# Optimization experiments

Measured on AMD Instinct MI355X. Metric: run time of the kernel, lower is better.

## Reference

```python
import jax, jax.numpy as jnp
import numpy as np

T = 8
TAU = 2.0
V_TH = 1.0
ALPHA = 2.0  # ATan surrogate alpha (spikingjelly default)

@jax.custom_vjp
def spike_fn(x):
    # Heaviside forward, ATan surrogate backward
    return (x >= 0.0).astype(x.dtype)

def _spike_fwd(x):
    return spike_fn(x), x

def _spike_bwd(x, g):
    sg = (ALPHA / 2.0) / (1.0 + (jnp.pi / 2.0 * ALPHA * x) ** 2)
    return (g * sg,)

spike_fn.defvjp(_spike_fwd, _spike_bwd)

def lif_scan(currents):
    """LIF over time. currents: (T, B, D). tau=2, v_reset=0 (hard), decay_input=True, detach_reset=True."""
    v0 = jnp.zeros(currents.shape[1:], currents.dtype)
    def step(v, x):
        v = v + (x - v) / TAU            # charge with input decay
        s = spike_fn(v - V_TH)           # fire
        sd = jax.lax.stop_gradient(s)    # detach_reset=True
        v = v * (1.0 - sd)               # hard reset to v_reset=0
        return v, s
    _, spikes = jax.lax.scan(step, v0, currents)
    return spikes  # (T, B, D)

def _linear(x, W, b):
    # x: (T,B,I), W: (O,I) torch layout
    return jnp.einsum('tbi,oi->tbo', x, W) + b

def setup_inputs() -> dict:
    key = jax.random.key(0)
    ks = jax.random.split(key, 9)
    B, D_in, D_out = 32768, 128, 64
    def lin(k, o, i):
        k1, k2 = jax.random.split(k)
        bound = 1.0 / np.sqrt(i)
        W = jax.random.uniform(k1, (o, i), jnp.float32, -bound, bound)
        b = jax.random.uniform(k2, (o,), jnp.float32, -bound, bound)
        return W, b
    W1, b1 = lin(ks[1], 256, D_in)
    W2, b2 = lin(ks[2], 128, 256)
    W3, b3 = lin(ks[3], 64, 128)
    W4, b4 = lin(ks[4], D_out, 64)
    x = jax.random.normal(ks[0], (B, D_in), jnp.float32)
    return {"x": x, "W1": W1, "b1": b1, "W2": W2, "b2": b2,
            "W3": W3, "b3": b3, "W4": W4, "b4": b4}

def reference(x, W1, b1, W2, b2, W3, b3, W4, b4):
    # Poisson rate coding: bernoulli(sigmoid(x)) per timestep (fixed key => deterministic)
    p = jax.nn.sigmoid(x)
    enc_key = jax.random.key(42)
    spikes_in = jax.random.bernoulli(enc_key, p, (T,) + x.shape).astype(x.dtype)  # (T,B,128)
    h = lif_scan(_linear(spikes_in, W1, b1))
    h = lif_scan(_linear(h, W2, b2))
    h = lif_scan(_linear(h, W3, b3))
    out = _linear(h, W4, b4)  # (T,B,64)
    return out.mean(axis=0)   # (B,64)
```

## Files before the change

### kernel.cpp

```cpp
#include <hip/hip_runtime.h>
#include <hip/hip_bf16.h>
#include <stdint.h>
#include <math.h>

#define TT 8

typedef __attribute__((ext_vector_type(8))) short short8;
typedef __attribute__((ext_vector_type(4))) float f32x4;

__device__ __forceinline__ uint16_t bf16_rne(float f) {
  uint32_t u = __float_as_uint(f);
  return (uint16_t)((u + 0x7fffu + ((u >> 16) & 1u)) >> 16);
}
__device__ __forceinline__ float bf16_f32(uint16_t b) {
  return __uint_as_float((uint32_t)b << 16);
}

__device__ __forceinline__ uint32_t rotl32(uint32_t v, int r) {
#if __has_builtin(__builtin_amdgcn_alignbit)
  return __builtin_amdgcn_alignbit(v, v, 32 - r);
#else
  return (v << r) | (v >> (32 - r));
#endif
}

__device__ __forceinline__ void tf_0_42(uint32_t x0, uint32_t x1,
                                        uint32_t& o0, uint32_t& o1) {
  const uint32_t K1 = 42u, KS2 = 0x1BD11BDAu ^ 42u;
  uint32_t v0 = x0;
  uint32_t v1 = x1 + K1;
#define R4(a,b,c,d) \
  v0 += v1; v1 = rotl32(v1, a); v1 ^= v0; \
  v0 += v1; v1 = rotl32(v1, b); v1 ^= v0; \
  v0 += v1; v1 = rotl32(v1, c); v1 ^= v0; \
  v0 += v1; v1 = rotl32(v1, d); v1 ^= v0;
  R4(13, 15, 26, 6)   v0 += K1;  v1 += KS2 + 1u;
  R4(17, 29, 16, 24)  v0 += KS2; v1 += 2u;
  R4(13, 15, 26, 6)   v1 += K1 + 3u;
  R4(17, 29, 16, 24)  v0 += K1;  v1 += KS2 + 4u;
  R4(13, 15, 26, 6)   v0 += KS2; v1 += 5u;
#undef R4
  o0 = v0; o1 = v1;
}

__device__ __forceinline__ void threefry2x32(uint32_t k0, uint32_t k1,
                                             uint32_t x0, uint32_t x1,
                                             uint32_t& o0, uint32_t& o1) {
  const uint32_t ks2 = 0x1BD11BDAu ^ k0 ^ k1;
  uint32_t v0 = x0 + k0, v1 = x1 + k1;
#define TFR(r) { v0 += v1; v1 = rotl32(v1, r); v1 ^= v0; }
  TFR(13) TFR(15) TFR(26) TFR(6)   v0 += k1;  v1 += ks2 + 1u;
  TFR(17) TFR(29) TFR(16) TFR(24)  v0 += ks2; v1 += k0 + 2u;
  TFR(13) TFR(15) TFR(26) TFR(6)   v0 += k0;  v1 += k1 + 3u;
  TFR(17) TFR(29) TFR(16) TFR(24)  v0 += k1;  v1 += ks2 + 4u;
  TFR(13) TFR(15) TFR(26) TFR(6)   v0 += ks2; v1 += k0 + 5u;
#undef TFR
  o0 = v0; o1 = v1;
}

__device__ __forceinline__ bool bern_lt(uint32_t bits, float p32, float xv) {
  const float u = __uint_as_float((bits >> 9) | 0x3f800000u) - 1.0f;
  const float d = u - p32;
  if (__builtin_expect(fabsf(d) < 8e-6f, 0)) {
    const double p = 1.0 / (1.0 + exp(-(double)xv));
    return (double)u < p;
  }
  return d < 0.0f;
}

__global__ void __launch_bounds__(256)
w1split_kernel(const float* __restrict__ W1, uint16_t* __restrict__ W1s)
{
  const int gid = blockIdx.x * 256 + threadIdx.x;
  const int j = gid & 7, nt = (gid >> 3) & 1, lane = (gid >> 4) & 63;
  const int sp = (gid >> 10) & 3, nc = gid >> 12;
  const int k = sp * 32 + (lane >> 4) * 8 + j;
  const int n = nc * 32 + nt * 16 + (lane & 15);
  W1s[gid] = bf16_rne(W1[n * 128 + k]);
}

__global__ void __launch_bounds__(256, 6)
snn_k1(const float* __restrict__ x, const uint16_t* __restrict__ W1s,
       const float* __restrict__ B1, const float* __restrict__ B4,
       uint32_t* __restrict__ s1g, uint32_t* __restrict__ flgg,
       float* __restrict__ out)
{
  __shared__ __align__(16) uint8_t sbits[128 * 16];
  __shared__ float bias_s[256];
  __shared__ uint16_t s1t[128 * 16];
  __shared__ uint32_t exc;

  const int tid = threadIdx.x;
  const int lane = tid & 63, wid = tid >> 6, g = lane >> 4;

  for (int i = tid; i < 1024; i += 256) ((uint32_t*)s1t)[i] = 0;
  if (tid == 0) exc = 0;
  bias_s[tid] = B1[tid];

  {
    const int b = tid >> 4, w8 = tid & 15;
    const int gb = blockIdx.x * 16 + b;
    float xv[8];
    *(float4*)&xv[0] = *(const float4*)&x[(size_t)gb * 128 + w8 * 8];
    *(float4*)&xv[4] = *(const float4*)&x[(size_t)gb * 128 + w8 * 8 + 4];
    const uint32_t ebase = ((uint32_t)gb << 7) | (uint32_t)(w8 * 8);
    uint32_t m[TT] = {0, 0, 0, 0, 0, 0, 0, 0};
    uint32_t ambig = 0;
    #pragma unroll
    for (int j = 0; j < 8; ++j) {
      const float p1 = 1.0f + 1.0f / (1.0f + expf(-xv[j]));
      uint32_t T = (__float_as_uint(p1) & 0x7fffffu) << 9;
      if (p1 >= 2.0f) T = 0xFFFFFFFFu;
      #pragma unroll
      for (int t = 0; t < 4; ++t) {
        const uint32_t e = ebase + (uint32_t)j + ((uint32_t)t << 22);
        uint32_t o0, o1;
        tf_0_42(e, e + 0x01000000u, o0, o1);
        m[t]     |= (o0 < T ? 1u : 0u) << j;
        m[t + 4] |= (o1 < T ? 1u : 0u) << j;
        const uint32_t a0 = o0 - T + 43008u, a1 = o1 - T + 43008u;
        ambig |= ((a0 < 86016u) || (a1 < 86016u)) ? (1u << j) : 0u;
      }
    }
    if (__builtin_expect(ambig != 0u, 0)) {
      for (int j = 0; j < 8; ++j) {
        if ((ambig >> j) & 1u) {
          const double p = 1.0 / (1.0 + exp(-(double)xv[j]));
          for (int t = 0; t < 4; ++t) {
            const uint32_t e = ebase + (uint32_t)j + ((uint32_t)t << 22);
            uint32_t o0, o1;
            tf_0_42(e, e + 0x01000000u, o0, o1);
            const float u0 = __uint_as_float((o0 >> 9) | 0x3f800000u) - 1.0f;
            const float u1 = __uint_as_float((o1 >> 9) | 0x3f800000u) - 1.0f;
            m[t]     = (m[t]     & ~(1u << j)) | (((double)u0 < p ? 1u : 0u) << j);
            m[t + 4] = (m[t + 4] & ~(1u << j)) | (((double)u1 < p ? 1u : 0u) << j);
          }
        }
      }
    }
    #pragma unroll
    for (int t = 0; t < TT; ++t)
      sbits[(b * 8 + t) * 16 + w8] = (uint8_t)m[t];
  }
  __syncthreads();

  short8 a0_0, a0_1, a0_2, a0_3, a1_0, a1_1, a1_2, a1_3;
  {
    const uint8_t* rp0 = &sbits[(wid * 32 + (lane & 15)) * 16];
    const uint8_t* rp1 = rp0 + 256;
#define MKFRAG(dst, rp, s) { \
    const uint32_t byte = (rp)[(s) * 4 + g]; \
    short8 a; \
    a[0] = (short)((byte & 1u)   ? 0x3F80 : 0); \
    a[1] = (short)((byte & 2u)   ? 0x3F80 : 0); \
    a[2] = (short)((byte & 4u)   ? 0x3F80 : 0); \
    a[3] = (short)((byte & 8u)   ? 0x3F80 : 0); \
    a[4] = (short)((byte & 16u)  ? 0x3F80 : 0); \
    a[5] = (short)((byte & 32u)  ? 0x3F80 : 0); \
    a[6] = (short)((byte & 64u)  ? 0x3F80 : 0); \
    a[7] = (short)((byte & 128u) ? 0x3F80 : 0); \
    dst = a; }
    MKFRAG(a0_0, rp0, 0) MKFRAG(a0_1, rp0, 1) MKFRAG(a0_2, rp0, 2) MKFRAG(a0_3, rp0, 3)
    MKFRAG(a1_0, rp1, 0) MKFRAG(a1_1, rp1, 1) MKFRAG(a1_2, rp1, 2) MKFRAG(a1_3, rp1, 3)
#undef MKFRAG
  }

  const uint8_t* wlane = (const uint8_t*)W1s + lane * 32;

  #pragma unroll 1
  for (int nc = 0; nc < 8; ++nc) {
    const uint8_t* wnc = wlane + nc * 8192;
    f32x4 C00 = {0.f, 0.f, 0.f, 0.f};
    f32x4 C01 = C00, C10 = C00, C11 = C00;
    short8 bf0, bf1;
#define STEP(sp, A0, A1) \
    bf0 = *(const short8*)(wnc + (sp) * 2048); \
    bf1 = *(const short8*)(wnc + (sp) * 2048 + 16); \
    C00 = __builtin_amdgcn_mfma_f32_16x16x32_bf16(A0, bf0, C00, 0, 0, 0); \
    C10 = __builtin_amdgcn_mfma_f32_16x16x32_bf16(A1, bf0, C10, 0, 0, 0); \
    C01 = __builtin_amdgcn_mfma_f32_16x16x32_bf16(A0, bf1, C01, 0, 0, 0); \
    C11 = __builtin_amdgcn_mfma_f32_16x16x32_bf16(A1, bf1, C11, 0, 0, 0);
    STEP(0, a0_0, a1_0) STEP(1, a0_1, a1_1) STEP(2, a0_2, a1_2) STEP(3, a0_3, a1_3)
#undef STEP

#define EPI(Cv, mi, nt) { \
    const float bbv = bias_s[nc * 32 + (nt) * 16 + (lane & 15)]; \
    const float cr0 = Cv[0] + bbv, cr1 = Cv[1] + bbv; \
    const float cr2 = Cv[2] + bbv, cr3 = Cv[3] + bbv; \
    float u = cr0 * 0.5f; \
    float mx = u; \
    u = (u + cr1) * 0.5f; mx = fmaxf(mx, u); \
    u = (u + cr2) * 0.5f; mx = fmaxf(mx, u); \
    u = (u + cr3) * 0.5f; mx = fmaxf(mx, u); \
    const float u3o = __shfl_xor(u, 16); \
    const float ub = (g & 1) ? mx + fmaxf(u3o, 0.f) * 0.5f : mx; \
    if (__any(ub >= 1.0f)) { \
      float v = 0.f; uint32_t nib = 0; \
      { const float vn = (v + cr0) * 0.5f; const bool s = vn >= 1.0f; nib |= s ? 1u : 0u; v = s ? 0.f : vn; } \
      { const float vn = (v + cr1) * 0.5f; const bool s = vn >= 1.0f; nib |= s ? 2u : 0u; v = s ? 0.f : vn; } \
      { const float vn = (v + cr2) * 0.5f; const bool s = vn >= 1.0f; nib |= s ? 4u : 0u; v = s ? 0.f : vn; } \
      { const float vn = (v + cr3) * 0.5f; const bool s = vn >= 1.0f; nib |= s ? 8u : 0u; v = s ? 0.f : vn; } \
      const float v3 = __shfl_xor(v, 16); \
      if (g & 1) { \
        v = v3; nib = 0; \
        { const float vn = (v + cr0) * 0.5f; const bool s = vn >= 1.0f; nib |= s ? 1u : 0u; v = s ? 0.f : vn; } \
        { const float vn = (v + cr1) * 0.5f; const bool s = vn >= 1.0f; nib |= s ? 2u : 0u; v = s ? 0.f : vn; } \
        { const float vn = (v + cr2) * 0.5f; const bool s = vn >= 1.0f; nib |= s ? 4u : 0u; v = s ? 0.f : vn; } \
        { const float vn = (v + cr3) * 0.5f; const bool s = vn >= 1.0f; nib |= s ? 8u : 0u; v = s ? 0.f : vn; } \
      } \
      _Pragma("unroll") \
      for (int r = 0; r < 4; ++r) { \
        const unsigned long long bal = __ballot((nib >> r) & 1u); \
        if ((lane & 15) == 0) { \
          const uint16_t w16v = (uint16_t)((bal >> (g * 16)) & 0xffffu); \
          if (w16v) { \
            const int row = wid * 32 + (mi) * 16 + g * 4 + r; \
            s1t[row * 16 + nc * 2 + (nt)] = w16v; \
          } \
        } \
      } \
    } }
    EPI(C00, 0, 0) EPI(C01, 0, 1) EPI(C10, 1, 0) EPI(C11, 1, 1)
#undef EPI
  }

  __syncthreads();
  if (tid < 128) {
    const uint32_t* rp = (const uint32_t*)&s1t[tid * 16];
    int c = 0;
    #pragma unroll
    for (int j = 0; j < 8; ++j) c += __popc(rp[j]);
    if (c >= 15) atomicOr(&exc, 1u);
  }
  ((uint4*)s1g)[(size_t)blockIdx.x * 256 + tid] = ((const uint4*)s1t)[tid];
  __syncthreads();
  const uint32_t e = exc;
  if (tid == 0) flgg[blockIdx.x] = e;
  if (!e) {
    const float4 bv = *reinterpret_cast<const float4*>(&B4[(tid & 15) * 4]);
    float* op = &out[(size_t)(blockIdx.x * 16 + (tid >> 4)) * 64 + (tid & 15) * 4];
    *reinterpret_cast<float4*>(op) = bv;
  }
}

template<int I, int O, bool LAST>
__device__ __forceinline__ void layer_valu(
    const float* __restrict__ Wg, const float* __restrict__ Bg,
    const uint32_t* __restrict__ s_in, uint8_t* __restrict__ s_out,
    uint32_t* __restrict__ flg_next,
    float* __restrict__ wbuf, float* __restrict__ bias_s,
    float* __restrict__ outp, int bglob0, uint32_t msk)
{
  constexpr int WST = 66;
  const int tid = threadIdx.x;
  const int b  = tid >> 3;
  const int oc = tid & 7;
  __syncthreads();
  if (tid < O) bias_s[tid] = Bg[tid];

  for (int q = 0; q < O / 64; ++q) {
    const int obase = q * 64;
    float acc[TT][8];
    #pragma unroll
    for (int t = 0; t < TT; ++t)
      #pragma unroll
      for (int j = 0; j < 8; ++j) acc[t][j] = 0.f;

    for (int ic = 0; ic < I / 64; ++ic) {
      if (!((msk >> ic) & 1u)) continue;
      __syncthreads();
      #pragma unroll
      for (int k = 0; k < 4; ++k) {
        int fi = tid + k * 256;
        int o  = fi >> 4;
        int i4 = fi & 15;
        const float4 w4 = *reinterpret_cast<const float4*>(
            &Wg[(size_t)(obase + o) * I + ic * 64 + i4 * 4]);
        float* wp = &wbuf[(i4 * 4) * WST + o];
        wp[0 * WST] = w4.x; wp[1 * WST] = w4.y;
        wp[2 * WST] = w4.z; wp[3 * WST] = w4.w;
      }
      __syncthreads();
      uint32_t r[TT][2];
      uint32_t any = 0;
      #pragma unroll
      for (int t = 0; t < TT; ++t) {
        const uint32_t* sp = &s_in[(size_t)(b * 8 + t) * (I / 32) + ic * 2];
        r[t][0] = sp[0]; r[t][1] = sp[1];
        any |= r[t][0] | r[t][1];
      }
      if (any) {
        #pragma unroll
        for (int w = 0; w < 2; ++w) {
          for (int i2 = 0; i2 < 32; ++i2) {
            const float* wrow = &wbuf[(w * 32 + i2) * WST + oc * 8];
            const float2 wa = *reinterpret_cast<const float2*>(wrow);
            const float2 wb = *reinterpret_cast<const float2*>(wrow + 2);
            const float2 wc = *reinterpret_cast<const float2*>(wrow + 4);
            const float2 wd = *reinterpret_cast<const float2*>(wrow + 6);
            #pragma unroll
            for (int t = 0; t < TT; ++t) {
              const float sf = (float)((r[t][w] >> i2) & 1u);
              acc[t][0] += wa.x * sf; acc[t][1] += wa.y * sf;
              acc[t][2] += wb.x * sf; acc[t][3] += wb.y * sf;
              acc[t][4] += wc.x * sf; acc[t][5] += wc.y * sf;
              acc[t][6] += wd.x * sf; acc[t][7] += wd.y * sf;
            }
          }
        }
      }
    }
    if constexpr (!LAST) {
      float v[8];
      #pragma unroll
      for (int j = 0; j < 8; ++j) v[j] = 0.f;
      #pragma unroll
      for (int t = 0; t < TT; ++t) {
        uint32_t m = 0;
        #pragma unroll
        for (int j = 0; j < 8; ++j) {
          const float cur = acc[t][j] + bias_s[obase + oc * 8 + j];
          const float vn = (v[j] + cur) * 0.5f;
          const bool s = vn >= 1.0f;
          m |= (uint32_t)s << j;
          v[j] = s ? 0.0f : vn;
        }
        if (m) {
          const int byi = (obase >> 3) + oc;
          s_out[(size_t)(b * 8 + t) * (O / 8) + byi] = (uint8_t)m;
          atomicOr(flg_next, 1u << (byi >> 3));
        }
      }
    } else {
      float oacc[8];
      #pragma unroll
      for (int j = 0; j < 8; ++j) oacc[j] = 0.f;
      #pragma unroll
      for (int t = 0; t < TT; ++t)
        #pragma unroll
        for (int j = 0; j < 8; ++j) oacc[j] += acc[t][j];
      float4 o0, o1;
      o0.x = oacc[0] * 0.125f + bias_s[oc * 8 + 0];
      o0.y = oacc[1] * 0.125f + bias_s[oc * 8 + 1];
      o0.z = oacc[2] * 0.125f + bias_s[oc * 8 + 2];
      o0.w = oacc[3] * 0.125f + bias_s[oc * 8 + 3];
      o1.x = oacc[4] * 0.125f + bias_s[oc * 8 + 4];
      o1.y = oacc[5] * 0.125f + bias_s[oc * 8 + 5];
      o1.z = oacc[6] * 0.125f + bias_s[oc * 8 + 6];
      o1.w = oacc[7] * 0.125f + bias_s[oc * 8 + 7];
      float* op = &outp[(size_t)(bglob0 + b) * 64 + oc * 8];
      *reinterpret_cast<float4*>(op)     = o0;
      *reinterpret_cast<float4*>(op + 4) = o1;
    }
  }
}

__global__ void __launch_bounds__(256, 4)
snn_k2(const uint32_t* __restrict__ s1g, const uint32_t* __restrict__ flgg,
       const float* __restrict__ W2, const float* __restrict__ B2,
       const float* __restrict__ W3, const float* __restrict__ B3,
       const float* __restrict__ W4, const float* __restrict__ B4,
       float* __restrict__ out)
{
  const uint32_t m1 = flgg[2 * blockIdx.x] | flgg[2 * blockIdx.x + 1];
  if (!m1) return;

  __shared__ __align__(16) uint8_t smem[32272];
  float*    wbuf   = (float*)smem;
  float*    bias_s = (float*)(smem + 16896);
  uint8_t*  s2     = smem + 17920;
  uint32_t* s1     = (uint32_t*)(smem + 22016);
  uint8_t*  s3     = smem + 30208;
  uint32_t* flg    = (uint32_t*)(smem + 32256);

  const int tid = threadIdx.x;
  const int bglob0 = blockIdx.x * 32;

  ((uint4*)s1)[tid]       = ((const uint4*)s1g)[(size_t)blockIdx.x * 512 + tid];
  ((uint4*)s1)[tid + 256] = ((const uint4*)s1g)[(size_t)blockIdx.x * 512 + tid + 256];
  for (int i = tid; i < 1024; i += 256) ((uint32_t*)s2)[i] = 0;
  for (int i = tid; i < 516;  i += 256) ((uint32_t*)s3)[i] = 0;

  layer_valu<256, 128, false>(W2, B2, s1, s2, &flg[1],
                              wbuf, bias_s, nullptr, bglob0, 0xFu);
  __syncthreads();
  const uint32_t m2 = flg[1];
  if (m2)
    layer_valu<128, 64, false>(W3, B3, (const uint32_t*)s2, s3, &flg[2],
                               wbuf, bias_s, nullptr, bglob0, m2);
  __syncthreads();
  const uint32_t m3 = flg[2];
  if (m3) {
    layer_valu<64, 64, true>(W4, B4, (const uint32_t*)s3, nullptr, nullptr,
                             wbuf, bias_s, out, bglob0, m3);
  } else {
    const int b = tid >> 3, oc = tid & 7;
    const float4 b0 = *reinterpret_cast<const float4*>(&B4[oc * 8]);
    const float4 b1 = *reinterpret_cast<const float4*>(&B4[oc * 8 + 4]);
    float* op = &out[(size_t)(bglob0 + b) * 64 + oc * 8];
    *reinterpret_cast<float4*>(op)     = b0;
    *reinterpret_cast<float4*>(op + 4) = b1;
  }
}

__global__ void __launch_bounds__(256, 4)
snn_fb(const float* __restrict__ x,
       const float* __restrict__ W1, const float* __restrict__ B1,
       const float* __restrict__ W2, const float* __restrict__ B2,
       const float* __restrict__ W3, const float* __restrict__ B3,
       const float* __restrict__ W4, const float* __restrict__ B4,
       float* __restrict__ out)
{
  __shared__ __align__(16) uint8_t smem[32272];
  uint16_t* B_lds  = (uint16_t*)smem;
  float*    wbuf   = (float*)smem;
  float*    bias_s = (float*)(smem + 16896);
  uint32_t* s0     = (uint32_t*)(smem + 17920);
  uint8_t*  s2     = smem + 17920;
  uint16_t* s1     = (uint16_t*)(smem + 22016);
  uint8_t*  s3     = smem + 30208;
  uint32_t* flg    = (uint32_t*)(smem + 32256);

  const int tid = threadIdx.x;
  const int lane = tid & 63, wid = tid >> 6;
  const int bglob0 = blockIdx.x * 32;

  for (int i = tid; i < 2564; i += 256)
    ((uint32_t*)(smem + 22016))[i] = 0;

  {
    const int b = tid >> 3, w16 = tid & 7;
    const int gb = bglob0 + b;
    float xv[16];
    #pragma unroll
    for (int k = 0; k < 4; ++k)
      *(float4*)&xv[k * 4] =
          *(const float4*)&x[(size_t)gb * 128 + w16 * 16 + k * 4];
    uint32_t m[TT] = {0, 0, 0, 0, 0, 0, 0, 0};
    for (int j = 0; j < 16; ++j) {
      const int d = w16 * 16 + j;
      const float p32 = 1.0f / (1.0f + expf(-xv[j]));
      #pragma unroll
      for (int t = 0; t < 4; ++t) {
        const uint32_t e = ((uint32_t)t << 22) | ((uint32_t)gb << 7) | (uint32_t)d;
        uint32_t o0, o1;
        threefry2x32(0u, 42u, e, e + 0x01000000u, o0, o1);
        m[t]     |= (uint32_t)bern_lt(o0, p32, xv[j]) << j;
        m[t + 4] |= (uint32_t)bern_lt(o1, p32, xv[j]) << j;
      }
    }
    #pragma unroll
    for (int t = 0; t < TT; ++t)
      ((uint16_t*)s0)[(b * 8 + t) * 8 + w16] = (uint16_t)m[t];
  }
  bias_s[tid] = B1[tid];
  __syncthreads();

  short8 afrag[4][4];
  #pragma unroll
  for (int m = 0; m < 4; ++m) {
    const int row = wid * 64 + m * 16 + (lane & 15);
    #pragma unroll
    for (int s = 0; s < 4; ++s) {
      const uint32_t wrd = s0[row * 4 + s];
      const uint32_t byte = (wrd >> ((lane >> 4) * 8)) & 0xffu;
      short8 a;
      #pragma unroll
      for (int j = 0; j < 8; ++j)
        a[j] = (short)(((byte >> j) & 1u) ? 0x3F80 : 0);
      afrag[m][s] = a;
    }
  }
  __syncthreads();
  for (int i = tid; i < 1024; i += 256)
    ((uint32_t*)s2)[i] = 0;

  for (int nc = 0; nc < 8; ++nc) {
    __syncthreads();
    {
      const int col = tid >> 3, kq = tid & 7;
      const float* wsrc = &W1[(size_t)(nc * 32 + col) * 128 + kq * 16];
      float4 f[4];
      #pragma unroll
      for (int k = 0; k < 4; ++k)
        f[k] = *reinterpret_cast<const float4*>(wsrc + k * 4);
      #pragma unroll
      for (int h = 0; h < 2; ++h) {
        const int k0 = kq * 16 + h * 8;
        const int sp = k0 >> 5, gg = (k0 >> 3) & 3;
        short8 hv, lv;
        #pragma unroll
        for (int e = 0; e < 8; ++e) {
          const float w = ((const float*)&f[2 * h])[e];
          const uint16_t hb = bf16_rne(w);
          const uint16_t lb = bf16_rne(w - bf16_f32(hb));
          hv[e] = (short)hb; lv[e] = (short)lb;
        }
        *(short8*)(B_lds + ((sp * 4 + gg) * 33 + col) * 8)       = hv;
        *(short8*)(B_lds + (((sp + 4) * 4 + gg) * 33 + col) * 8) = lv;
      }
    }
    __syncthreads();
    f32x4 C[4][2];
    #pragma unroll
    for (int m = 0; m < 4; ++m)
      #pragma unroll
      for (int nt = 0; nt < 2; ++nt)
        C[m][nt] = (f32x4){0.f, 0.f, 0.f, 0.f};
    #pragma unroll
    for (int nt = 0; nt < 2; ++nt)
      #pragma unroll
      for (int sp = 0; sp < 8; ++sp) {
        const short8 bf = *(const short8*)(
            B_lds + ((sp * 4 + (lane >> 4)) * 33 + nt * 16 + (lane & 15)) * 8);
        #pragma unroll
        for (int m = 0; m < 4; ++m)
          C[m][nt] = __builtin_amdgcn_mfma_f32_16x16x32_bf16(
              afrag[m][sp & 3], bf, C[m][nt], 0, 0, 0);
      }
    const int g = lane >> 4;
    #pragma unroll
    for (int m = 0; m < 4; ++m)
      #pragma unroll
      for (int nt = 0; nt < 2; ++nt) {
        const float bb = bias_s[nc * 32 + nt * 16 + (lane & 15)];
        const float c0 = C[m][nt][0] + bb, c1 = C[m][nt][1] + bb;
        const float c2 = C[m][nt][2] + bb, c3 = C[m][nt][3] + bb;
        const float mxc = fmaxf(fmaxf(c0, c1), fmaxf(c2, c3));
        if (__any(mxc >= 1.0f)) {
          float cr[4] = {c0, c1, c2, c3};
          float v = 0.f; uint32_t nib = 0;
          #pragma unroll
          for (int r = 0; r < 4; ++r) {
            const float vn = (v + cr[r]) * 0.5f;
            const bool s = vn >= 1.0f;
            nib |= (uint32_t)s << r;
            v = s ? 0.f : vn;
          }
          const float v3 = __shfl_xor(v, 16);
          if (g & 1) {
            v = v3; nib = 0;
            #pragma unroll
            for (int r = 0; r < 4; ++r) {
              const float vn = (v + cr[r]) * 0.5f;
              const bool s = vn >= 1.0f;
              nib |= (uint32_t)s << r;
              v = s ? 0.f : vn;
            }
          }
          #pragma unroll
          for (int r = 0; r < 4; ++r) {
            const unsigned long long bal = __ballot((nib >> r) & 1u);
            if ((lane & 15) == 0) {
              const uint16_t w16v = (uint16_t)((bal >> (g * 16)) & 0xffffu);
              if (w16v) {
                const int row = wid * 64 + m * 16 + g * 4 + r;
                const int wds = nc * 2 + nt;
                s1[row * 16 + wds] = w16v;
                atomicOr(&flg[0], 1u << (wds >> 2));
              }
            }
          }
        }
      }
  }

  __syncthreads();
  const uint32_t m1 = flg[0];
  if (m1)
    layer_valu<256, 128, false>(W2, B2, (const uint32_t*)s1, s2, &flg[1],
                                wbuf, bias_s, nullptr, bglob0, m1);
  __syncthreads();
  const uint32_t m2 = flg[1];
  if (m2)
    layer_valu<128, 64, false>(W3, B3, (const uint32_t*)s2, s3, &flg[2],
                               wbuf, bias_s, nullptr, bglob0, m2);
  __syncthreads();
  const uint32_t m3 = flg[2];
  if (m3) {
    layer_valu<64, 64, true>(W4, B4, (const uint32_t*)s3, nullptr, nullptr,
                             wbuf, bias_s, out, bglob0, m3);
  } else {
    const int b = tid >> 3, oc = tid & 7;
    const float4 b0 = *reinterpret_cast<const float4*>(&B4[oc * 8]);
    const float4 b1 = *reinterpret_cast<const float4*>(&B4[oc * 8 + 4]);
    float* op = &out[(size_t)(bglob0 + b) * 64 + oc * 8];
    *reinterpret_cast<float4*>(op)     = b0;
    *reinterpret_cast<float4*>(op + 4) = b1;
  }
}

extern "C" void kernel_launch(void* const* d_in, const int* in_sizes, int n_in,
                              void* d_out, int out_size, void* d_ws, size_t ws_size,
                              hipStream_t stream) {
  const float* x  = (const float*)d_in[0];
  const float* W1 = (const float*)d_in[1];
  const float* B1 = (const float*)d_in[2];
  const float* W2 = (const float*)d_in[3];
  const float* B2 = (const float*)d_in[4];
  const float* W3 = (const float*)d_in[5];
  const float* B3 = (const float*)d_in[6];
  const float* W4 = (const float*)d_in[7];
  const float* B4 = (const float*)d_in[8];
  float* out = (float*)d_out;
  const size_t s1_bytes  = (size_t)262144 * 32;
  const size_t flg_bytes = 2048 * 4;
  const size_t w1s_bytes = 32768 * 2;
  if (ws_size >= s1_bytes + flg_bytes + w1s_bytes) {
    uint32_t* s1g  = (uint32_t*)d_ws;
    uint32_t* flgg = (uint32_t*)((uint8_t*)d_ws + s1_bytes);
    uint16_t* W1s  = (uint16_t*)((uint8_t*)d_ws + s1_bytes + flg_bytes);
    hipLaunchKernelGGL(w1split_kernel, dim3(128), dim3(256), 0, stream, W1, W1s);
    hipLaunchKernelGGL(snn_k1, dim3(2048), dim3(256), 0, stream,
                       x, W1s, B1, B4, s1g, flgg, out);
    hipLaunchKernelGGL(snn_k2, dim3(1024), dim3(256), 0, stream,
                       s1g, flgg, W2, B2, W3, B3, W4, B4, out);
  } else {
    hipLaunchKernelGGL(snn_fb, dim3(1024), dim3(256), 0, stream,
                       x, W1, B1, W2, B2, W3, B3, W4, B4, out);
  }
}
```

Before: 77.39 us.

## Make snn_k1 wave-independent with register bpermute fragments and per-wave flags

Rewrites the first kernel so each wavefront handles its own 4 batch rows end to end. Bernoulli spike masks stay in registers and are redistributed into MFMA A-fragments with ds_bpermute instead of going through shared memory. The block-wide syncs and shared atomic for the overflow flag are replaced by a per-wave ballot and a per-wave flag array, which snn_k2 now ORs over 8 entries. Work is also remapped so each lane handles 32 inputs at one timestep pair, __expf replaces expf, and the occupancy hint drops from 6 to 4 blocks, which may reduce latency hiding.

```diff
diff --git a/kernel.cpp b/kernel.cpp
--- a/kernel.cpp
+++ b/kernel.cpp
@@ -79,77 +79,76 @@
   W1s[gid] = bf16_rne(W1[n * 128 + k]);
 }
 
-__global__ void __launch_bounds__(256, 6)
+__global__ void __launch_bounds__(256, 4)
 snn_k1(const float* __restrict__ x, const uint16_t* __restrict__ W1s,
        const float* __restrict__ B1, const float* __restrict__ B4,
        uint32_t* __restrict__ s1g, uint32_t* __restrict__ flgg,
        float* __restrict__ out)
 {
-  __shared__ __align__(16) uint8_t sbits[128 * 16];
   __shared__ float bias_s[256];
-  __shared__ uint16_t s1t[128 * 16];
-  __shared__ uint32_t exc;
+  __shared__ __align__(16) uint16_t s1t[4 * 512];
 
   const int tid = threadIdx.x;
   const int lane = tid & 63, wid = tid >> 6, g = lane >> 4;
-
-  for (int i = tid; i < 1024; i += 256) ((uint32_t*)s1t)[i] = 0;
-  if (tid == 0) exc = 0;
+  uint16_t* const s1w = &s1t[wid * 512];
+
   bias_s[tid] = B1[tid];
-
   {
-    const int b = tid >> 4, w8 = tid & 15;
-    const int gb = blockIdx.x * 16 + b;
-    float xv[8];
-    *(float4*)&xv[0] = *(const float4*)&x[(size_t)gb * 128 + w8 * 8];
-    *(float4*)&xv[4] = *(const float4*)&x[(size_t)gb * 128 + w8 * 8 + 4];
-    const uint32_t ebase = ((uint32_t)gb << 7) | (uint32_t)(w8 * 8);
-    uint32_t m[TT] = {0, 0, 0, 0, 0, 0, 0, 0};
-    uint32_t ambig = 0;
-    #pragma unroll
-    for (int j = 0; j < 8; ++j) {
-      const float p1 = 1.0f + 1.0f / (1.0f + expf(-xv[j]));
+    const uint4 z = {0, 0, 0, 0};
+    ((uint4*)s1w)[lane] = z;
+  }
+  __syncthreads();
+
+  const int s_loc = lane >> 4;
+  const int dg = (lane >> 2) & 3;
+  const int tp = lane & 3;
+  const int gb = blockIdx.x * 16 + wid * 4 + s_loc;
+  const float* xrow = &x[(size_t)gb * 128 + dg * 32];
+  const uint32_t ebase = ((uint32_t)tp << 22) | ((uint32_t)gb << 7) |
+                         (uint32_t)(dg * 32);
+  uint32_t m_lo = 0, m_hi = 0, amb = 0;
+  #pragma unroll
+  for (int dc = 0; dc < 4; ++dc) {
+    const float4 xa = *(const float4*)(xrow + dc * 8);
+    const float4 xb = *(const float4*)(xrow + dc * 8 + 4);
+    const float xs[8] = {xa.x, xa.y, xa.z, xa.w, xb.x, xb.y, xb.z, xb.w};
+    #pragma unroll
+    for (int jj = 0; jj < 8; ++jj) {
+      const float p1 = 1.0f + 1.0f / (1.0f + __expf(-xs[jj]));
       uint32_t T = (__float_as_uint(p1) & 0x7fffffu) << 9;
       if (p1 >= 2.0f) T = 0xFFFFFFFFu;
-      #pragma unroll
-      for (int t = 0; t < 4; ++t) {
-        const uint32_t e = ebase + (uint32_t)j + ((uint32_t)t << 22);
+      const uint32_t Tm = T - 43008u;
+      const int bit = dc * 8 + jj;
+      const uint32_t e = ebase + (uint32_t)bit;
+      uint32_t o0, o1;
+      tf_0_42(e, e + 0x01000000u, o0, o1);
+      m_lo |= (o0 < T ? 1u : 0u) << bit;
+      m_hi |= (o1 < T ? 1u : 0u) << bit;
+      amb  |= (((o0 - Tm) < 86016u) || ((o1 - Tm) < 86016u)) ? (1u << bit) : 0u;
+    }
+  }
+  if (__builtin_expect(amb != 0u, 0)) {
+    for (int bit = 0; bit < 32; ++bit) {
+      if ((amb >> bit) & 1u) {
+        const double p = 1.0 / (1.0 + exp(-(double)xrow[bit]));
+        const uint32_t e = ebase + (uint32_t)bit;
         uint32_t o0, o1;
         tf_0_42(e, e + 0x01000000u, o0, o1);
-        m[t]     |= (o0 < T ? 1u : 0u) << j;
-        m[t + 4] |= (o1 < T ? 1u : 0u) << j;
-        const uint32_t a0 = o0 - T + 43008u, a1 = o1 - T + 43008u;
-        ambig |= ((a0 < 86016u) || (a1 < 86016u)) ? (1u << j) : 0u;
+        const float u0 = __uint_as_float((o0 >> 9) | 0x3f800000u) - 1.0f;
+        const float u1 = __uint_as_float((o1 >> 9) | 0x3f800000u) - 1.0f;
+        m_lo = (m_lo & ~(1u << bit)) | (((double)u0 < p ? 1u : 0u) << bit);
+        m_hi = (m_hi & ~(1u << bit)) | (((double)u1 < p ? 1u : 0u) << bit);
       }
     }
-    if (__builtin_expect(ambig != 0u, 0)) {
-      for (int j = 0; j < 8; ++j) {
-        if ((ambig >> j) & 1u) {
-          const double p = 1.0 / (1.0 + exp(-(double)xv[j]));
-          for (int t = 0; t < 4; ++t) {
-            const uint32_t e = ebase + (uint32_t)j + ((uint32_t)t << 22);
-            uint32_t o0, o1;
-            tf_0_42(e, e + 0x01000000u, o0, o1);
-            const float u0 = __uint_as_float((o0 >> 9) | 0x3f800000u) - 1.0f;
-            const float u1 = __uint_as_float((o1 >> 9) | 0x3f800000u) - 1.0f;
-            m[t]     = (m[t]     & ~(1u << j)) | (((double)u0 < p ? 1u : 0u) << j);
-            m[t + 4] = (m[t + 4] & ~(1u << j)) | (((double)u1 < p ? 1u : 0u) << j);
-          }
-        }
-      }
-    }
-    #pragma unroll
-    for (int t = 0; t < TT; ++t)
-      sbits[(b * 8 + t) * 16 + w8] = (uint8_t)m[t];
-  }
-  __syncthreads();
+  }
 
   short8 a0_0, a0_1, a0_2, a0_3, a1_0, a1_1, a1_2, a1_3;
-  {
-    const uint8_t* rp0 = &sbits[(wid * 32 + (lane & 15)) * 16];
-    const uint8_t* rp1 = rp0 + 256;
-#define MKFRAG(dst, rp, s) { \
-    const uint32_t byte = (rp)[(s) * 4 + g]; \
+#define MKF(dst, mi, s) { \
+    const int src = ((((mi) * 2 + ((lane >> 3) & 1)) * 16 + (s) * 4 + (lane & 3))) * 4; \
+    const uint32_t wlo = (uint32_t)__builtin_amdgcn_ds_bpermute(src, (int)m_lo); \
+    const uint32_t whi = (uint32_t)__builtin_amdgcn_ds_bpermute(src, (int)m_hi); \
+    const uint32_t wsel = (lane & 4) ? whi : wlo; \
+    const uint32_t byte = (wsel >> (g * 8)) & 0xffu; \
     short8 a; \
     a[0] = (short)((byte & 1u)   ? 0x3F80 : 0); \
     a[1] = (short)((byte & 2u)   ? 0x3F80 : 0); \
@@ -160,10 +159,9 @@
     a[6] = (short)((byte & 64u)  ? 0x3F80 : 0); \
     a[7] = (short)((byte & 128u) ? 0x3F80 : 0); \
     dst = a; }
-    MKFRAG(a0_0, rp0, 0) MKFRAG(a0_1, rp0, 1) MKFRAG(a0_2, rp0, 2) MKFRAG(a0_3, rp0, 3)
-    MKFRAG(a1_0, rp1, 0) MKFRAG(a1_1, rp1, 1) MKFRAG(a1_2, rp1, 2) MKFRAG(a1_3, rp1, 3)
-#undef MKFRAG
-  }
+  MKF(a0_0, 0, 0) MKF(a0_1, 0, 1) MKF(a0_2, 0, 2) MKF(a0_3, 0, 3)
+  MKF(a1_0, 1, 0) MKF(a1_1, 1, 1) MKF(a1_2, 1, 2) MKF(a1_3, 1, 3)
+#undef MKF
 
   const uint8_t* wlane = (const uint8_t*)W1s + lane * 32;
 
@@ -214,8 +212,8 @@
         if ((lane & 15) == 0) { \
           const uint16_t w16v = (uint16_t)((bal >> (g * 16)) & 0xffffu); \
           if (w16v) { \
-            const int row = wid * 32 + (mi) * 16 + g * 4 + r; \
-            s1t[row * 16 + nc * 2 + (nt)] = w16v; \
+            const int row = (mi) * 16 + g * 4 + r; \
+            s1w[row * 16 + nc * 2 + (nt)] = w16v; \
           } \
         } \
       } \
@@ -224,21 +222,18 @@
 #undef EPI
   }
 
-  __syncthreads();
-  if (tid < 128) {
-    const uint32_t* rp = (const uint32_t*)&s1t[tid * 16];
-    int c = 0;
-    #pragma unroll
-    for (int j = 0; j < 8; ++j) c += __popc(rp[j]);
-    if (c >= 15) atomicOr(&exc, 1u);
-  }
-  ((uint4*)s1g)[(size_t)blockIdx.x * 256 + tid] = ((const uint4*)s1t)[tid];
-  __syncthreads();
-  const uint32_t e = exc;
-  if (tid == 0) flgg[blockIdx.x] = e;
-  if (!e) {
-    const float4 bv = *reinterpret_cast<const float4*>(&B4[(tid & 15) * 4]);
-    float* op = &out[(size_t)(blockIdx.x * 16 + (tid >> 4)) * 64 + (tid & 15) * 4];
+  const int rr = lane & 31;
+  const uint4 w0 = ((const uint4*)s1w)[rr * 2];
+  const uint4 w1 = ((const uint4*)s1w)[rr * 2 + 1];
+  int c = __popc(w0.x) + __popc(w0.y) + __popc(w0.z) + __popc(w0.w) +
+          __popc(w1.x) + __popc(w1.y) + __popc(w1.z) + __popc(w1.w);
+  const bool exc = __ballot((lane < 32) && (c >= 15)) != 0ull;
+  ((uint4*)s1g)[(size_t)blockIdx.x * 256 + wid * 64 + lane] = ((const uint4*)s1w)[lane];
+  if (lane == 0) flgg[blockIdx.x * 4 + wid] = exc ? 1u : 0u;
+  if (!exc) {
+    const float4 bv = ((const float4*)B4)[lane & 15];
+    float* op = &out[(size_t)(blockIdx.x * 16 + wid * 4 + (lane >> 4)) * 64 +
+                     (lane & 15) * 4];
     *reinterpret_cast<float4*>(op) = bv;
   }
 }
@@ -362,7 +357,9 @@
        const float* __restrict__ W4, const float* __restrict__ B4,
        float* __restrict__ out)
 {
-  const uint32_t m1 = flgg[2 * blockIdx.x] | flgg[2 * blockIdx.x + 1];
+  const uint32_t* fp = &flgg[(size_t)blockIdx.x * 8];
+  const uint32_t m1 = fp[0] | fp[1] | fp[2] | fp[3] |
+                      fp[4] | fp[5] | fp[6] | fp[7];
   if (!m1) return;
 
   __shared__ __align__(16) uint8_t smem[32272];
@@ -604,7 +601,7 @@
   const float* B4 = (const float*)d_in[8];
   float* out = (float*)d_out;
   const size_t s1_bytes  = (size_t)262144 * 32;
-  const size_t flg_bytes = 2048 * 4;
+  const size_t flg_bytes = 2048 * 4 * 4;
   const size_t w1s_bytes = 32768 * 2;
   if (ws_size >= s1_bytes + flg_bytes + w1s_bytes) {
     uint32_t* s1g  = (uint32_t*)d_ws;
```

New measurement: 80.70 us. 1.04x slower.
